# Kernel tuning notes

Hardware: AMD Instinct MI355X
Metric: run time of the kernel (lower is better)

## Reference

```python
import jax, jax.numpy as jnp
import numpy as np

C, S, D, H, FF = 8, 512, 512, 8, 2048
DH = D // H
N = C * S
NUM_SAMPLES = 4
SEG_LEN = N // NUM_SAMPLES  # 2 channels * 512 tokens per sample


def _ln(x, w, b):
    m = x.mean(-1, keepdims=True)
    v = ((x - m) ** 2).mean(-1, keepdims=True)
    return (x - m) / jnp.sqrt(v + 1e-5) * w + b


def _rope_1d(t, p, inv_freq):
    # t: (H, N, hd), p: (N,), inv_freq: (hd//2,)
    f = p[:, None] * inv_freq[None, :]          # (N, hd//2)
    emb = jnp.concatenate([f, f], -1)           # (N, hd)
    cos, sin = jnp.cos(emb), jnp.sin(emb)
    half = t.shape[-1] // 2
    rot = jnp.concatenate([-t[..., half:], t[..., :half]], -1)
    return t * cos + rot * sin


def setup_inputs() -> dict:
    key = jax.random.key(0)
    ks = jax.random.split(key, 8)
    s = 0.02
    return {
        "x": jax.random.normal(ks[0], (C, S, D), jnp.float32),
        "pos": jax.random.uniform(ks[1], (C, S, 2), jnp.float32) * 100.0,
        "mask": jnp.zeros((C, S), jnp.bool_),
        "seg_ids": jnp.arange(N, dtype=jnp.int32),
        "Wqkv": jax.random.normal(ks[2], (D, 3 * D), jnp.float32) * s,
        "bqkv": jnp.zeros((3 * D,), jnp.float32),
        "Wo": jax.random.normal(ks[3], (D, D), jnp.float32) * s,
        "bo": jnp.zeros((D,), jnp.float32),
        "ln1_w": jnp.ones((D,), jnp.float32),
        "ln1_b": jnp.zeros((D,), jnp.float32),
        "ln2_w": jnp.ones((D,), jnp.float32),
        "ln2_b": jnp.zeros((D,), jnp.float32),
        "W1": jax.random.normal(ks[4], (D, FF), jnp.float32) * s,
        "b1": jnp.zeros((FF,), jnp.float32),
        "W2": jax.random.normal(ks[5], (FF, D), jnp.float32) * s,
        "b2": jnp.zeros((D,), jnp.float32),
    }


def reference(x, pos, mask, seg_ids, Wqkv, bqkv, Wo, bo,
              ln1_w, ln1_b, ln2_w, ln2_b, W1, b1, W2, b2):
    # Zero-mask forward_cc path: all C*S tokens are packed into one varlen batch.
    xf = x.reshape(N, D)
    pf = pos.reshape(N, 2)
    seg = seg_ids // SEG_LEN  # segment id per token (cu_seq_len semantics)

    # --- pre-LN MHA with 2D axial RoPE ---
    hn = _ln(xf, ln1_w, ln1_b)
    qkv = hn @ Wqkv + bqkv
    q, k, v = jnp.split(qkv, 3, axis=-1)
    to_heads = lambda t: t.reshape(N, H, DH).transpose(1, 0, 2)  # (H, N, DH)
    q, k, v = to_heads(q), to_heads(k), to_heads(v)

    hd2 = DH // 2
    inv_freq = 1.0 / (10000.0 ** (jnp.arange(0, hd2, 2, dtype=jnp.float32) / hd2))

    def rope2d(t):
        a = _rope_1d(t[..., :hd2], pf[:, 0], inv_freq)
        b = _rope_1d(t[..., hd2:], pf[:, 1], inv_freq)
        return jnp.concatenate([a, b], -1)

    q, k = rope2d(q), rope2d(k)

    scores = jnp.einsum('hnd,hmd->hnm', q, k) / np.float32(np.sqrt(DH))
    allowed = seg[:, None] == seg[None, :]  # block-diagonal varlen mask
    scores = jnp.where(allowed[None], scores, jnp.float32(-1e30))
    attn = jax.nn.softmax(scores, axis=-1)
    o = jnp.einsum('hnm,hmd->hnd', attn, v).transpose(1, 0, 2).reshape(N, D)
    h = xf + (o @ Wo + bo)

    # --- pre-LN FFN ---
    hn2 = _ln(h, ln2_w, ln2_b)
    h = h + (jax.nn.gelu(hn2 @ W1 + b1) @ W2 + b2)
    return h.reshape(C, S, D)
```

## Files before the change

### kernel.cpp

```cpp
#include <hip/hip_runtime.h>
#include <hip/hip_bf16.h>


typedef __hip_bfloat16 bf16;
typedef float f4 __attribute__((ext_vector_type(4)));
typedef short short8 __attribute__((ext_vector_type(8)));

#define C_ 8
#define S_ 512
#define D_ 512
#define H_ 8
#define DH_ 64
#define FF_ 2048
#define N_ 4096
#define SEGLEN 1024

__device__ __forceinline__ float bfbits2f(unsigned short u) {
    return __uint_as_float(((unsigned)u) << 16);
}
__device__ __forceinline__ unsigned short f2bfbits(float f) {
    __hip_bfloat16 h = __float2bfloat16(f);
    return *reinterpret_cast<unsigned short*>(&h);
}
__device__ __forceinline__ float in_get(const void* p, int i, int isbf) {
    return isbf ? bfbits2f(((const unsigned short*)p)[i]) : ((const float*)p)[i];
}
__device__ __forceinline__ int probe_bf(const void* ln1w) {
    return ((const unsigned*)ln1w)[0] != 0x3F800000u;
}
__device__ __forceinline__ float gelu_f(float x) {
    float u = 0.7978845608028654f * fmaf(0.044715f * x, x * x, x);
    return 0.5f * x * (1.0f + tanhf(u));
}
__device__ __forceinline__ void gl2lds16(const void* g, void* l) {
    __builtin_amdgcn_global_load_lds(
        (const __attribute__((address_space(1))) void*)g,
        (__attribute__((address_space(3))) void*)l, 16, 0, 0);
}

__device__ __forceinline__ void ln_row(
    const void* in, const void* w, const void* b, unsigned short* out,
    int isbf, int row, int lane, int in_fp32)
{
    int base = row * D_ + lane * 8;
    float v[8];
    if (in_fp32 || !isbf) {
        const f4* p = (const f4*)((const float*)in + base);
        f4 x0 = p[0], x1 = p[1];
        v[0] = x0[0]; v[1] = x0[1]; v[2] = x0[2]; v[3] = x0[3];
        v[4] = x1[0]; v[5] = x1[1]; v[6] = x1[2]; v[7] = x1[3];
    } else {
        uint4 u = *(const uint4*)((const unsigned short*)in + base);
        unsigned uu[4] = {u.x, u.y, u.z, u.w};
        #pragma unroll
        for (int j = 0; j < 4; j++) {
            v[2 * j]     = __uint_as_float(uu[j] << 16);
            v[2 * j + 1] = __uint_as_float(uu[j] & 0xFFFF0000u);
        }
    }
    float s = 0.f, q = 0.f;
    #pragma unroll
    for (int j = 0; j < 8; j++) { s += v[j]; q = fmaf(v[j], v[j], q); }
    #pragma unroll
    for (int m = 32; m; m >>= 1) { s += __shfl_xor(s, m); q += __shfl_xor(q, m); }
    float mean = s * (1.f / D_);
    float var  = q * (1.f / D_) - mean * mean;
    float rstd = rsqrtf(var + 1e-5f);
    unsigned short o[8];
    #pragma unroll
    for (int j = 0; j < 8; j++) {
        float wj = in_get(w, lane * 8 + j, isbf);
        float bj = in_get(b, lane * 8 + j, isbf);
        o[j] = f2bfbits((v[j] - mean) * rstd * wj + bj);
    }
    uint4 uo;
    uo.x = o[0] | ((unsigned)o[1] << 16);
    uo.y = o[2] | ((unsigned)o[3] << 16);
    uo.z = o[4] | ((unsigned)o[5] << 16);
    uo.w = o[6] | ((unsigned)o[7] << 16);
    *(uint4*)(out + base) = uo;
}

__device__ __forceinline__ void wtile_transpose(
    const void* __restrict__ src, bf16* __restrict__ dst, int K, int N,
    int nt, int kt, int isbf, unsigned short* t2)
{
    int nb = nt * 64, kb = kt * 32;
    #pragma unroll
    for (int pass = 0; pass < 2; pass++) {
        int k = pass * 16 + (threadIdx.x >> 4);
        int n = (threadIdx.x & 15) * 4;
        size_t gidx = (size_t)(kb + k) * N + nb + n;
        unsigned short v[4];
        if (!isbf) {
            f4 xv = *(const f4*)((const float*)src + gidx);
            v[0] = f2bfbits(xv[0]); v[1] = f2bfbits(xv[1]);
            v[2] = f2bfbits(xv[2]); v[3] = f2bfbits(xv[3]);
        } else {
            ushort4 u = *(const ushort4*)((const unsigned short*)src + gidx);
            v[0] = u.x; v[1] = u.y; v[2] = u.z; v[3] = u.w;
        }
        #pragma unroll
        for (int e = 0; e < 4; e++) t2[(n + e) * 40 + k] = v[e];
    }
    __syncthreads();
    int n = threadIdx.x >> 2, kc = (threadIdx.x & 3) * 8;
    uint4 w = *(const uint4*)&t2[n * 40 + kc];
    *(uint4*)&((unsigned short*)dst)[(size_t)(nb + n) * K + kb + kc] = w;
}

__global__ __launch_bounds__(256) void prep_kernel(
    const void* __restrict__ Wqkv, bf16* __restrict__ WqkvT,
    const void* __restrict__ x, const void* __restrict__ ln1w,
    const void* __restrict__ ln1b, unsigned short* __restrict__ hn)
{
    const int isbf = probe_bf(ln1w);
    __shared__ unsigned short t2[64 * 40];
    int b = blockIdx.x;
    if (b < 384) {
        wtile_transpose(Wqkv, WqkvT, 512, 1536, b % 24, b / 24, isbf, t2);
    } else {
        int row = (b - 384) * 4 + (threadIdx.x >> 6);
        ln_row(x, ln1w, ln1b, hn, isbf, row, threadIdx.x & 63, 0);
    }
}

__global__ __launch_bounds__(256) void ln_kernel(
    const void* __restrict__ in, const void* __restrict__ w, const void* __restrict__ b,
    unsigned short* __restrict__ out, const void* __restrict__ dtp, int in_fp32)
{
    const int isbf = probe_bf(dtp);
    int row = blockIdx.x * 4 + (threadIdx.x >> 6);
    ln_row(in, w, b, out, isbf, row, threadIdx.x & 63, in_fp32);
}

template<int MODE, int TM, int TN>
__global__ __launch_bounds__(256) void gemm_kernel(
    const bf16* __restrict__ A, const bf16* __restrict__ Bt,
    const void* __restrict__ bias, const void* __restrict__ res,
    const void* __restrict__ pos,
    void* __restrict__ out0, void* __restrict__ out1,
    int K, int NN, const void* __restrict__ dtp)
{
    const int isbf = probe_bf(dtp);
    constexpr int MI = TM / 32;
    constexpr int NT = TN / 32;
    constexpr int NB = TN / 32;
    constexpr int AS = TM * 64;
    constexpr int BS = TN * 64;
    constexpr int BUF = AS + BS;
    constexpr int VTSZ = 128 * 72;
    constexpr int SMSZ = (2 * BUF > VTSZ) ? 2 * BUF : VTSZ;
    __shared__ __align__(16) unsigned short smem[SMSZ];

    const int X = blockIdx.x & 7, jj = blockIdx.x >> 3;
    const int m0 = ((jj / NN) * 8 + X) * TM;
    const int n0 = (jj % NN) * TN;
    const int tid = threadIdx.x;
    const int wave = tid >> 6, lane = tid & 63;
    const int quad = lane >> 4, l16 = lane & 15;
    const int wr = wave >> 1, wc = wave & 1;

    const bf16* gA[MI]; int dA[MI];
    const bf16* gB[NB]; int dB[NB];
    #pragma unroll
    for (int j = 0; j < MI; j++) {
        int s = j * 256 + tid;
        int r = s >> 3, cc = ((s & 7) - r) & 7;
        gA[j] = A + (size_t)(m0 + r) * K + cc * 8;
        dA[j] = (j * 256 + wave * 64) * 8;
    }
    #pragma unroll
    for (int j = 0; j < NB; j++) {
        int s = j * 256 + tid;
        int r = s >> 3, cc = ((s & 7) - r) & 7;
        gB[j] = Bt + (size_t)(n0 + r) * K + cc * 8;
        dB[j] = (j * 256 + wave * 64) * 8;
    }
    auto stage = [&](int b, int kt) {
        unsigned short* Ab = smem + b * BUF;
        unsigned short* Bb = Ab + AS;
        #pragma unroll
        for (int j = 0; j < MI; j++) gl2lds16(gA[j] + kt * 64, Ab + dA[j]);
        #pragma unroll
        for (int j = 0; j < NB; j++) gl2lds16(gB[j] + kt * 64, Bb + dB[j]);
    };

    f4 acc[MI][NT] = {};
    const int nk = K >> 6;
    stage(0, 0);
    #pragma unroll 1
    for (int kt = 0; kt < nk; kt++) {
        const int cur = kt & 1;
        __syncthreads();
        if (kt + 1 < nk) stage(cur ^ 1, kt + 1);
        const unsigned short* Ab = smem + cur * BUF;
        const unsigned short* Bb = Ab + AS;
        short8 af[MI][2], bfr[NT][2];
        #pragma unroll
        for (int mi = 0; mi < MI; mi++) {
            int r = wr * (TM / 2) + mi * 16 + l16;
            #pragma unroll
            for (int h = 0; h < 2; h++)
                af[mi][h] = *(const short8*)&Ab[(r * 8 + ((h * 4 + quad + r) & 7)) * 8];
        }
        #pragma unroll
        for (int ni = 0; ni < NT; ni++) {
            int r = wc * (TN / 2) + ni * 16 + l16;
            #pragma unroll
            for (int h = 0; h < 2; h++)
                bfr[ni][h] = *(const short8*)&Bb[(r * 8 + ((h * 4 + quad + r) & 7)) * 8];
        }
        #pragma unroll
        for (int mi = 0; mi < MI; mi++)
            #pragma unroll
            for (int ni = 0; ni < NT; ni++) {
                acc[mi][ni] = __builtin_amdgcn_mfma_f32_16x16x32_bf16(af[mi][0], bfr[ni][0], acc[mi][ni], 0, 0, 0);
                acc[mi][ni] = __builtin_amdgcn_mfma_f32_16x16x32_bf16(af[mi][1], bfr[ni][1], acc[mi][ni], 0, 0, 0);
            }
    }

    const int colbase = n0 + wc * (TN / 2);
    float bb[NT];
    #pragma unroll
    for (int ni = 0; ni < NT; ni++) bb[ni] = in_get(bias, colbase + ni * 16 + l16, isbf);

    if (MODE == 1) {
        const int tsel = colbase >> 9;
        const int hd = (colbase & 511) >> 6;
        if (tsel < 2) {
            unsigned short* out = (unsigned short*)out0 + ((size_t)(tsel * H_ + hd) * N_) * 64;
            const float invf = __expf(-(float)l16 * 0.5756462732485114f);
            const float qscale = (tsel == 0) ? 0.125f : 1.0f;
            #pragma unroll
            for (int half = 0; half < 2; half++) {
                #pragma unroll
                for (int mi = 0; mi < MI; mi++) {
                    #pragma unroll
                    for (int r = 0; r < 4; r++) {
                        int row = m0 + wr * (TM / 2) + mi * 16 + quad * 4 + r;
                        float p = in_get(pos, row * 2 + half, isbf);
                        float sn, cs;
                        __sincosf(p * invf, &sn, &cs);
                        float v0 = acc[mi][half * 2][r]     + bb[half * 2];
                        float v1 = acc[mi][half * 2 + 1][r] + bb[half * 2 + 1];
                        out[(size_t)row * 64 + half * 32 + l16]      = f2bfbits((v0 * cs - v1 * sn) * qscale);
                        out[(size_t)row * 64 + half * 32 + 16 + l16] = f2bfbits((v1 * cs + v0 * sn) * qscale);
                    }
                }
            }
        } else {
            __syncthreads();
            unsigned short* VT = smem;
            const int vd_blk = n0 - 1024;
            #pragma unroll
            for (int mi = 0; mi < MI; mi++)
                #pragma unroll
                for (int ni = 0; ni < NT; ni++) {
                    int vd = wc * 64 + ni * 16 + l16;
                    #pragma unroll
                    for (int r = 0; r < 4; r++) {
                        int tok = wr * (TM / 2) + mi * 16 + quad * 4 + r;
                        VT[vd * 72 + tok] = f2bfbits(acc[mi][ni][r] + bb[ni]);
                    }
                }
            __syncthreads();
            unsigned short* vt = (unsigned short*)out1;
            #pragma unroll
            for (int j = 0; j < 4; j++) {
                int cch = j * 256 + tid;
                int dim = cch >> 3, tc = cch & 7;
                uint4 v = *(const uint4*)&VT[dim * 72 + tc * 8];
                *(uint4*)&vt[(size_t)(vd_blk + dim) * N_ + m0 + tc * 8] = v;
            }
        }
    } else {
        #pragma unroll
        for (int mi = 0; mi < MI; mi++)
            #pragma unroll
            for (int ni = 0; ni < NT; ni++) {
                int col = colbase + ni * 16 + l16;
                #pragma unroll
                for (int r = 0; r < 4; r++) {
                    int row = m0 + wr * (TM / 2) + mi * 16 + quad * 4 + r;
                    float val = acc[mi][ni][r] + bb[ni];
                    if (MODE == 2) {
                        size_t idx = (size_t)row * D_ + col;
                        ((float*)out0)[idx] = val + in_get(res, idx, isbf);
                    } else if (MODE == 3) {
                        ((unsigned short*)out0)[(size_t)row * FF_ + col] = f2bfbits(gelu_f(val));
                    } else {
                        size_t idx = (size_t)row * D_ + col;
                        float o = val + ((const float*)res)[idx];
                        if (isbf) ((unsigned short*)out0)[idx] = f2bfbits(o);
                        else      ((float*)out0)[idx] = o;
                    }
                }
            }
    }
}

#define PSTR 136
__global__ __launch_bounds__(256) void attn_kernel(
    const unsigned short* __restrict__ QKb, const unsigned short* __restrict__ Vt,
    unsigned short* __restrict__ ob,
    const void* __restrict__ tWo, const void* __restrict__ tW1,
    const void* __restrict__ tW2,
    bf16* __restrict__ dWo, bf16* __restrict__ dW1, bf16* __restrict__ dW2,
    const void* __restrict__ dtp)
{
    __shared__ __align__(16) unsigned short Ksm[128 * 64];
    __shared__ __align__(16) unsigned short Vsm[64 * 128];
    __shared__ __align__(16) unsigned short Psm[4][16 * PSTR];

    if ((int)blockIdx.x >= 512) {
        const int isbf = probe_bf(dtp);
        int t = blockIdx.x - 512;
        if (t < 128)      wtile_transpose(tWo, dWo, 512, 512,  t % 8,  t / 8,  isbf, Ksm);
        else if (t < 640) wtile_transpose(tW1, dW1, 512, 2048, (t - 128) % 32, (t - 128) / 32, isbf, Ksm);
        else              wtile_transpose(tW2, dW2, 2048, 512, (t - 640) % 8,  (t - 640) / 8,  isbf, Ksm);
        return;
    }

    const int h = blockIdx.x & 7, jb = blockIdx.x >> 3;
    const int sg = jb >> 4, qt = jb & 15;
    const int tid = threadIdx.x;
    const int wave = tid >> 6, lane = tid & 63;
    const int quad = lane >> 4, l16 = lane & 15;
    const unsigned short* Qg = QKb + ((size_t)h * N_ + sg * SEGLEN + qt * 64 + wave * 16) * 64;
    const unsigned short* Kg = QKb + ((size_t)(H_ + h) * N_ + sg * SEGLEN) * 64;
    const unsigned short* Vg = Vt + (size_t)h * 64 * N_ + sg * SEGLEN;
    unsigned short* Pw = Psm[wave];

    const unsigned short* gK[4];
    const unsigned short* gV[4];
    unsigned short* lK[4];
    unsigned short* lV[4];
    #pragma unroll
    for (int j = 0; j < 4; j++) {
        int s = j * 256 + tid;
        int rk = s >> 3, ck = ((s & 7) - rk) & 7;
        gK[j] = Kg + (size_t)rk * 64 + ck * 8;
        lK[j] = Ksm + (size_t)(j * 256 + wave * 64) * 8;
        int rv = s >> 4, cv = ((s & 15) - rv) & 15;
        gV[j] = Vg + (size_t)rv * N_ + cv * 8;
        lV[j] = Vsm + (size_t)(j * 256 + wave * 64) * 8;
    }
    const int swzK0 = (quad + l16) & 7;
    const int swzK1 = (4 + quad + l16) & 7;
    int swzV[4];
    #pragma unroll
    for (int kc = 0; kc < 4; kc++) swzV[kc] = (kc * 4 + quad + l16) & 15;

    short8 qf0 = *(const short8*)(Qg + l16 * 64 + quad * 8);
    short8 qf1 = *(const short8*)(Qg + l16 * 64 + 32 + quad * 8);

    f4 o_acc[4] = {};
    float l_part[4] = {0.f, 0.f, 0.f, 0.f};

    #pragma unroll 1
    for (int kt = 0; kt < SEGLEN / 128; kt++) {
        __syncthreads();
        #pragma unroll
        for (int j = 0; j < 4; j++) {
            gl2lds16(gK[j] + (size_t)kt * 128 * 64, lK[j]);
            gl2lds16(gV[j] + kt * 128, lV[j]);
        }
        __syncthreads();

        f4 Sc[8] = {};
        #pragma unroll
        for (int t = 0; t < 8; t++) {
            int r = t * 16 + l16;
            short8 kf0 = *(const short8*)&Ksm[(r * 8 + swzK0) * 8];
            short8 kf1 = *(const short8*)&Ksm[(r * 8 + swzK1) * 8];
            Sc[t] = __builtin_amdgcn_mfma_f32_16x16x32_bf16(qf0, kf0, Sc[t], 0, 0, 0);
            Sc[t] = __builtin_amdgcn_mfma_f32_16x16x32_bf16(qf1, kf1, Sc[t], 0, 0, 0);
        }
        #pragma unroll
        for (int t = 0; t < 8; t++)
            #pragma unroll
            for (int r = 0; r < 4; r++) {
                float pe = __expf(Sc[t][r]);
                Sc[t][r] = pe;
                l_part[r] += pe;
            }
        #pragma unroll
        for (int t = 0; t < 8; t++)
            #pragma unroll
            for (int r = 0; r < 4; r++)
                Pw[(quad * 4 + r) * PSTR + t * 16 + l16] = f2bfbits(Sc[t][r]);
        short8 pf[4];
        #pragma unroll
        for (int kc = 0; kc < 4; kc++)
            pf[kc] = *(const short8*)&Pw[l16 * PSTR + kc * 32 + quad * 8];
        #pragma unroll
        for (int dt = 0; dt < 4; dt++) {
            int r = dt * 16 + l16;
            #pragma unroll
            for (int kc = 0; kc < 4; kc++) {
                short8 vf = *(const short8*)&Vsm[(r * 16 + swzV[kc]) * 8];
                o_acc[dt] = __builtin_amdgcn_mfma_f32_16x16x32_bf16(pf[kc], vf, o_acc[dt], 0, 0, 0);
            }
        }
    }

    #pragma unroll
    for (int r = 0; r < 4; r++) {
        float l = l_part[r];
        l += __shfl_xor(l, 1);
        l += __shfl_xor(l, 2);
        l += __shfl_xor(l, 4);
        l += __shfl_xor(l, 8);
        float inv = 1.0f / l;
        int n = sg * SEGLEN + qt * 64 + wave * 16 + quad * 4 + r;
        #pragma unroll
        for (int dt = 0; dt < 4; dt++)
            ob[(size_t)n * D_ + h * DH_ + dt * 16 + l16] = f2bfbits(o_acc[dt][r] * inv);
    }
}

extern "C" void kernel_launch(void* const* d_in, const int* in_sizes, int n_in,
                              void* d_out, int out_size, void* d_ws, size_t ws_size,
                              hipStream_t stream)
{
    const void* x    = d_in[0];
    const void* pos  = d_in[1];
    const void* Wqkv = d_in[4];
    const void* bqkv = d_in[5];
    const void* Wo   = d_in[6];
    const void* bo   = d_in[7];
    const void* ln1w = d_in[8];
    const void* ln1b = d_in[9];
    const void* ln2w = d_in[10];
    const void* ln2b = d_in[11];
    const void* W1   = d_in[12];
    const void* b1   = d_in[13];
    const void* W2   = d_in[14];
    const void* b2   = d_in[15];

    char* ws = (char*)d_ws;
    size_t off = 0;
    auto take = [&](size_t bytes) -> void* {
        void* p = ws + off;
        off += (bytes + 255) & ~(size_t)255;
        return p;
    };
    bf16* WqkvT           = (bf16*)take((size_t)1536 * 512 * 2);
    bf16* WoT             = (bf16*)take((size_t)512 * 512 * 2);
    bf16* W1T             = (bf16*)take((size_t)2048 * 512 * 2);
    bf16* W2T             = (bf16*)take((size_t)512 * 2048 * 2);
    unsigned short* hn    = (unsigned short*)take((size_t)N_ * D_ * 2);
    unsigned short* QKb   = (unsigned short*)take((size_t)2 * H_ * N_ * DH_ * 2);
    unsigned short* Vtb   = (unsigned short*)take((size_t)H_ * DH_ * N_ * 2);
    unsigned short* obuf  = (unsigned short*)take((size_t)N_ * D_ * 2);
    float* hbuf           = (float*)take((size_t)N_ * D_ * 4);
    unsigned short* hn2   = (unsigned short*)take((size_t)N_ * D_ * 2);
    unsigned short* g     = (unsigned short*)take((size_t)N_ * FF_ * 2);

    prep_kernel<<<1408, 256, 0, stream>>>(Wqkv, WqkvT, x, ln1w, ln1b, hn);

    gemm_kernel<1, 64, 128><<<768, 256, 0, stream>>>(
        (const bf16*)hn, WqkvT, bqkv, nullptr, pos, QKb, Vtb, 512, 12, ln1w);

    attn_kernel<<<1664, 256, 0, stream>>>(
        QKb, Vtb, obuf, Wo, W1, W2, WoT, W1T, W2T, ln1w);

    gemm_kernel<2, 32, 64><<<1024, 256, 0, stream>>>(
        (const bf16*)obuf, WoT, bo, x, nullptr, hbuf, nullptr, 512, 8, ln1w);

    ln_kernel<<<N_ / 4, 256, 0, stream>>>(hbuf, ln2w, ln2b, hn2, ln1w, 1);

    gemm_kernel<3, 64, 64><<<2048, 256, 0, stream>>>(
        (const bf16*)hn2, W1T, b1, nullptr, nullptr, g, nullptr, 512, 32, ln1w);

    gemm_kernel<4, 32, 64><<<1024, 256, 0, stream>>>(
        (const bf16*)g, W2T, b2, hbuf, nullptr, d_out, nullptr, 2048, 8, ln1w);
}
```

Measured before the change: 191.6 us.

## Double-buffer K tiles in attention, read V from global, cheaper GELU

The attention kernel now double-buffers the K tile in LDS. It prefetches the next tile with async global-to-LDS loads while the current one is computed, and uses one barrier per iteration instead of two. V is no longer staged in LDS; each lane reads its V fragments straight from the transposed global V array, which relies on cache hits and may add load latency inside the MFMA loop. GELU's tanh form is rewritten as an equivalent exp plus hardware-reciprocal expression, and the softmax normaliser uses the fast reciprocal, trading a little precision for fewer instructions.

```diff
diff --git a/kernel.cpp b/kernel.cpp
--- a/kernel.cpp
+++ b/kernel.cpp
@@ -30,7 +30,7 @@
 }
 __device__ __forceinline__ float gelu_f(float x) {
     float u = 0.7978845608028654f * fmaf(0.044715f * x, x * x, x);
-    return 0.5f * x * (1.0f + tanhf(u));
+    return x * __builtin_amdgcn_rcpf(1.0f + __expf(-2.0f * u));
 }
 __device__ __forceinline__ void gl2lds16(const void* g, void* l) {
     __builtin_amdgcn_global_load_lds(
@@ -309,16 +309,15 @@
     bf16* __restrict__ dWo, bf16* __restrict__ dW1, bf16* __restrict__ dW2,
     const void* __restrict__ dtp)
 {
-    __shared__ __align__(16) unsigned short Ksm[128 * 64];
-    __shared__ __align__(16) unsigned short Vsm[64 * 128];
+    __shared__ __align__(16) unsigned short Ksm[2][128 * 64];
     __shared__ __align__(16) unsigned short Psm[4][16 * PSTR];
 
     if ((int)blockIdx.x >= 512) {
         const int isbf = probe_bf(dtp);
         int t = blockIdx.x - 512;
-        if (t < 128)      wtile_transpose(tWo, dWo, 512, 512,  t % 8,  t / 8,  isbf, Ksm);
-        else if (t < 640) wtile_transpose(tW1, dW1, 512, 2048, (t - 128) % 32, (t - 128) / 32, isbf, Ksm);
-        else              wtile_transpose(tW2, dW2, 2048, 512, (t - 640) % 8,  (t - 640) / 8,  isbf, Ksm);
+        if (t < 128)      wtile_transpose(tWo, dWo, 512, 512,  t % 8,  t / 8,  isbf, Ksm[0]);
+        else if (t < 640) wtile_transpose(tW1, dW1, 512, 2048, (t - 128) % 32, (t - 128) / 32, isbf, Ksm[0]);
+        else              wtile_transpose(tW2, dW2, 2048, 512, (t - 640) % 8,  (t - 640) / 8,  isbf, Ksm[0]);
         return;
     }
 
@@ -329,28 +328,25 @@
     const int quad = lane >> 4, l16 = lane & 15;
     const unsigned short* Qg = QKb + ((size_t)h * N_ + sg * SEGLEN + qt * 64 + wave * 16) * 64;
     const unsigned short* Kg = QKb + ((size_t)(H_ + h) * N_ + sg * SEGLEN) * 64;
-    const unsigned short* Vg = Vt + (size_t)h * 64 * N_ + sg * SEGLEN;
     unsigned short* Pw = Psm[wave];
 
     const unsigned short* gK[4];
-    const unsigned short* gV[4];
-    unsigned short* lK[4];
-    unsigned short* lV[4];
+    int lKoff[4];
     #pragma unroll
     for (int j = 0; j < 4; j++) {
         int s = j * 256 + tid;
         int rk = s >> 3, ck = ((s & 7) - rk) & 7;
         gK[j] = Kg + (size_t)rk * 64 + ck * 8;
-        lK[j] = Ksm + (size_t)(j * 256 + wave * 64) * 8;
-        int rv = s >> 4, cv = ((s & 15) - rv) & 15;
-        gV[j] = Vg + (size_t)rv * N_ + cv * 8;
-        lV[j] = Vsm + (size_t)(j * 256 + wave * 64) * 8;
+        lKoff[j] = (j * 256 + wave * 64) * 8;
     }
     const int swzK0 = (quad + l16) & 7;
     const int swzK1 = (4 + quad + l16) & 7;
-    int swzV[4];
-    #pragma unroll
-    for (int kc = 0; kc < 4; kc++) swzV[kc] = (kc * 4 + quad + l16) & 15;
+
+    const unsigned short* Vp[4];
+    #pragma unroll
+    for (int dt = 0; dt < 4; dt++)
+        Vp[dt] = Vt + (size_t)h * 64 * N_ + (size_t)(dt * 16 + l16) * N_
+                    + sg * SEGLEN + quad * 8;
 
     short8 qf0 = *(const short8*)(Qg + l16 * 64 + quad * 8);
     short8 qf1 = *(const short8*)(Qg + l16 * 64 + 32 + quad * 8);
@@ -358,22 +354,26 @@
     f4 o_acc[4] = {};
     float l_part[4] = {0.f, 0.f, 0.f, 0.f};
 
+    #pragma unroll
+    for (int j = 0; j < 4; j++) gl2lds16(gK[j], &Ksm[0][lKoff[j]]);
+
     #pragma unroll 1
     for (int kt = 0; kt < SEGLEN / 128; kt++) {
+        const int cur = kt & 1;
         __syncthreads();
-        #pragma unroll
-        for (int j = 0; j < 4; j++) {
-            gl2lds16(gK[j] + (size_t)kt * 128 * 64, lK[j]);
-            gl2lds16(gV[j] + kt * 128, lV[j]);
-        }
-        __syncthreads();
+        if (kt + 1 < SEGLEN / 128) {
+            #pragma unroll
+            for (int j = 0; j < 4; j++)
+                gl2lds16(gK[j] + (size_t)(kt + 1) * 128 * 64, &Ksm[cur ^ 1][lKoff[j]]);
+        }
+        const unsigned short* Kb = Ksm[cur];
 
         f4 Sc[8] = {};
         #pragma unroll
         for (int t = 0; t < 8; t++) {
             int r = t * 16 + l16;
-            short8 kf0 = *(const short8*)&Ksm[(r * 8 + swzK0) * 8];
-            short8 kf1 = *(const short8*)&Ksm[(r * 8 + swzK1) * 8];
+            short8 kf0 = *(const short8*)&Kb[(r * 8 + swzK0) * 8];
+            short8 kf1 = *(const short8*)&Kb[(r * 8 + swzK1) * 8];
             Sc[t] = __builtin_amdgcn_mfma_f32_16x16x32_bf16(qf0, kf0, Sc[t], 0, 0, 0);
             Sc[t] = __builtin_amdgcn_mfma_f32_16x16x32_bf16(qf1, kf1, Sc[t], 0, 0, 0);
         }
@@ -396,10 +396,9 @@
             pf[kc] = *(const short8*)&Pw[l16 * PSTR + kc * 32 + quad * 8];
         #pragma unroll
         for (int dt = 0; dt < 4; dt++) {
-            int r = dt * 16 + l16;
             #pragma unroll
             for (int kc = 0; kc < 4; kc++) {
-                short8 vf = *(const short8*)&Vsm[(r * 16 + swzV[kc]) * 8];
+                short8 vf = *(const short8*)(Vp[dt] + kt * 128 + kc * 32);
                 o_acc[dt] = __builtin_amdgcn_mfma_f32_16x16x32_bf16(pf[kc], vf, o_acc[dt], 0, 0, 0);
             }
         }
@@ -412,7 +411,7 @@
         l += __shfl_xor(l, 2);
         l += __shfl_xor(l, 4);
         l += __shfl_xor(l, 8);
-        float inv = 1.0f / l;
+        float inv = __builtin_amdgcn_rcpf(l);
         int n = sg * SEGLEN + qt * 64 + wave * 16 + quad * 4 + r;
         #pragma unroll
         for (int dt = 0; dt < 4; dt++)
```

Result: slower. 205.9 us (+7.5%).
